# Optimization experiments

Measured on AMD Instinct MI355X. Metric: run time of the kernel, lower is better.

Reference implementation:

```python
import jax, jax.numpy as jnp
import numpy as np

B, N, K_NBR = 8, 4096, 16
H1, H3 = 512, 64
NS = 24  # covariance neighborhood size (hardcoded in encode)


def _local_cov(pc, ns):
    # Vectorized equivalent of the per-point sliding-window covariance loop.
    Bv, Nv, D = pc.shape
    half = ns // 2
    offs = jnp.arange(-half, half + 1)              # window size ns+1 = 25
    idx = jnp.arange(Nv)[:, None] + offs            # [N, 25]
    valid = (idx >= 0) & (idx < Nv)
    nb = pc[:, jnp.clip(idx, 0, Nv - 1), :]         # [B, N, 25, D]
    vm = valid[None, :, :, None].astype(pc.dtype)
    cnt = valid.sum(-1).astype(pc.dtype)[None, :, None]  # actual window counts
    mean = (nb * vm).sum(2) / cnt                   # [B, N, D]
    cen = (nb - mean[:, :, None, :]) * vm           # mask after centering
    cov = jnp.einsum('bnwd,bnwe->bnde', cen, cen) / (ns - 1)  # torch divides by ns-1
    return cov.reshape(Bv, Nv, D * D)


def _gcn(h, src, dst, w, b):
    # torch_geometric GCNConv: add self-loops, sym-normalize, aggregate at dst.
    Nt = h.shape[0]
    loop = jnp.arange(Nt, dtype=src.dtype)
    s = jnp.concatenate([src, loop])
    d = jnp.concatenate([dst, loop])
    deg = jax.ops.segment_sum(jnp.ones_like(d, h.dtype), d, num_segments=Nt)
    dinv = jnp.where(deg > 0, jax.lax.rsqrt(deg), 0.0)
    hw = h @ w
    msg = (dinv[s] * dinv[d])[:, None] * hw[s]
    return jax.ops.segment_sum(msg, d, num_segments=Nt) + b


def setup_inputs() -> dict:
    key = jax.random.key(0)
    ks = jax.random.split(key, 10)

    def lin(k, fi, fo):
        w = jax.random.normal(k, (fi, fo), jnp.float32) / np.float32(np.sqrt(fi))
        return w, jnp.zeros((fo,), jnp.float32)

    x = jax.random.normal(ks[0], (B, N, 3), jnp.float32)
    knn = jax.random.randint(ks[1], (2, B * N * K_NBR), 0, B * N, jnp.int32)
    w_e1, b_e1 = lin(ks[2], 12, H3)
    w_g1, b_g1 = lin(ks[3], H3, 2 * H3)
    w_g2, b_g2 = lin(ks[4], 2 * H3, H1)
    w_e2, b_e2 = lin(ks[5], H1, H1)
    w_d1, b_d1 = lin(ks[6], H1 + 2, 3)
    w_d2, b_d2 = lin(ks[7], H1 + 3, 3)
    return dict(x=x, knn=knn, w_e1=w_e1, b_e1=b_e1, w_g1=w_g1, b_g1=b_g1,
                w_g2=w_g2, b_g2=b_g2, w_e2=w_e2, b_e2=b_e2,
                w_d1=w_d1, b_d1=b_d1, w_d2=w_d2, b_d2=b_d2)


def reference(x, knn, w_e1, b_e1, w_g1, b_g1, w_g2, b_g2,
              w_e2, b_e2, w_d1, b_d1, w_d2, b_d2):
    act = jax.nn.selu
    Bv, Nv, _ = x.shape
    # ---- encode ----
    cov = _local_cov(x, NS)                                  # [B, N, 9]
    h = act(jnp.concatenate([x, cov], -1) @ w_e1 + b_e1)     # [B, N, H3]
    h = h.reshape(Bv * Nv, -1)
    h = act(_gcn(h, knn[0], knn[1], w_g1, b_g1))             # [B*N, 2*H3]
    h = act(_gcn(h, knn[0], knn[1], w_g2, b_g2))             # [B*N, H1]
    h = h.reshape(Bv, Nv, -1)
    lat = h.max(axis=1, keepdims=True)                       # AdaptiveMaxPool1d(1)
    lat = act(lat @ w_e2 + b_e2)                             # [B, 1, H1]
    # ---- decode ----
    nx = int(1 + (Nv * 120 / 60) ** 0.5)
    ny = int(1 + (Nv * 60 / 120) ** 0.5)
    xg = jnp.linspace(1.0, 120.0, nx)
    yg = jnp.linspace(1.0, 60.0, ny)
    grid = jnp.stack(jnp.meshgrid(xg, yg, indexing='ij'), -1).reshape(-1, 2)[:Nv]
    y = jnp.broadcast_to(grid[None], (Bv, Nv, 2))
    xr = jnp.broadcast_to(lat, (Bv, Nv, lat.shape[-1]))      # repeat codeword
    k = act(jnp.concatenate([xr, y], -1) @ w_d1 + b_d1)      # [B, N, 3]
    out = act(jnp.concatenate([xr, k], -1) @ w_d2 + b_d2)    # [B, N, 3]
    return out
```

## Files before the change

### kernel.cpp

```cpp
#include <hip/hip_runtime.h>
#include <math.h>

#define SELU_SCALE 1.0507009873554804934193349852946f
#define SELU_ALPHA 1.6732632423543772848170429916717f

typedef short bf16x8 __attribute__((ext_vector_type(8)));
typedef float f32x4 __attribute__((ext_vector_type(4)));

__device__ __forceinline__ float selu_f(float x) {
    return SELU_SCALE * (x > 0.f ? x : SELU_ALPHA * expm1f(x));
}

__device__ __forceinline__ unsigned short f2bf(float f) {
    unsigned int u = __float_as_uint(f);
    u += 0x7FFF + ((u >> 16) & 1);
    return (unsigned short)(u >> 16);
}
__device__ __forceinline__ float bflo(unsigned int u) { return __uint_as_float(u << 16); }
__device__ __forceinline__ float bfhi(unsigned int u) { return __uint_as_float(u & 0xFFFF0000u); }

__device__ __forceinline__ void acc8(float* a, uint4 v) {
    a[0] += bflo(v.x); a[1] += bfhi(v.x);
    a[2] += bflo(v.y); a[3] += bfhi(v.y);
    a[4] += bflo(v.z); a[5] += bfhi(v.z);
    a[6] += bflo(v.w); a[7] += bfhi(v.w);
}

__device__ __forceinline__ uint4 pack8(const float* a, float dv) {
    uint4 pk;
    pk.x = (unsigned int)f2bf(a[0] * dv) | ((unsigned int)f2bf(a[1] * dv) << 16);
    pk.y = (unsigned int)f2bf(a[2] * dv) | ((unsigned int)f2bf(a[3] * dv) << 16);
    pk.z = (unsigned int)f2bf(a[4] * dv) | ((unsigned int)f2bf(a[5] * dv) << 16);
    pk.w = (unsigned int)f2bf(a[6] * dv) | ((unsigned int)f2bf(a[7] * dv) << 16);
    return pk;
}

__global__ __launch_bounds__(256) void prep_kernel(
    int* __restrict__ cnt, unsigned int* __restrict__ pad1,
    unsigned int* __restrict__ pad2,
    const float* __restrict__ W1, unsigned short* __restrict__ Wp1,
    const float* __restrict__ W2, unsigned short* __restrict__ Wp2) {
    int b = blockIdx.x;
    int t = threadIdx.x;
    if (b < 128) {
        cnt[b * 256 + t] = 0;
    } else if (b == 128) {
        if (t < 32) pad1[t] = 0;
        if (t < 64) pad2[t] = 0;
    } else {
        if (t >= 64) return;
        int fb = b - 129;
        const float* W; unsigned short* Wp; int K, N, f;
        if (fb < 16) { W = W1; Wp = Wp1; K = 64; N = 128; f = fb; }
        else         { W = W2; Wp = Wp2; K = 128; N = 512; f = fb - 16; }
        int l = t;
        int KS = K / 32;
        int nt = f / KS, ks = f % KS;
        int ncol = nt * 16 + (l & 15);
        int k0 = ks * 32 + (l >> 4) * 8;
        unsigned short v[8];
        #pragma unroll
        for (int j = 0; j < 8; j++) v[j] = f2bf(W[(size_t)(k0 + j) * N + ncol]);
        *(uint4*)&Wp[((size_t)f * 64 + l) * 8] = *(uint4*)v;
    }
}

__global__ void count_kernel(const int* __restrict__ dst, int* __restrict__ cnt,
                             int* __restrict__ epos, int E) {
    int e = blockIdx.x * blockDim.x + threadIdx.x;
    if (e < E) epos[e] = atomicAdd(&cnt[dst[e]], 1);
}

__global__ __launch_bounds__(256) void scanA_kernel(const int* __restrict__ cnt,
                                                    int* __restrict__ blockSums) {
    __shared__ int red[256];
    int t = threadIdx.x;
    int c = cnt[blockIdx.x * 256 + t];
    red[t] = (c + 7) & ~7;
    __syncthreads();
    for (int s = 128; s > 0; s >>= 1) {
        if (t < s) red[t] += red[t + s];
        __syncthreads();
    }
    if (t == 0) blockSums[blockIdx.x] = red[0];
}

__global__ __launch_bounds__(256) void scanC_kernel(
    const int* __restrict__ cnt, const int* __restrict__ bsums,
    int* __restrict__ indptr, float* __restrict__ dinv, int* __restrict__ ssrc, int n) {
    __shared__ int sc[256];
    __shared__ int bs[128];
    int t = threadIdx.x;
    int ownSum = bsums[blockIdx.x];
    if (t < 128) bs[t] = bsums[t];
    int i = blockIdx.x * 256 + t;
    int c = cnt[i];
    int pc = (c + 7) & ~7;
    sc[t] = pc;
    __syncthreads();
    for (int off = 1; off < 128; off <<= 1) {
        int v = (t >= off && t < 128) ? bs[t - off] : 0;
        __syncthreads();
        if (t < 128) bs[t] += v;
        __syncthreads();
    }
    for (int off = 1; off < 256; off <<= 1) {
        int v = t >= off ? sc[t - off] : 0;
        __syncthreads();
        sc[t] += v;
        __syncthreads();
    }
    int blockOff = bs[blockIdx.x] - ownSum;
    int ip = blockOff + sc[t] - pc;
    indptr[i] = ip;
    dinv[i] = rsqrtf((float)(c + 1));
    for (int k = c; k < pc; k++) ssrc[ip + k] = n;
    if (i == n - 1) indptr[n] = blockOff + sc[t];
}

__global__ void scatter_kernel(const int* __restrict__ src, const int* __restrict__ dst,
                               const int* __restrict__ epos,
                               const int* __restrict__ indptr,
                               int* __restrict__ ssrc, int E) {
    int e = blockIdx.x * blockDim.x + threadIdx.x;
    if (e < E) ssrc[indptr[dst[e]] + epos[e]] = src[e];
}

__global__ __launch_bounds__(256) void cov_enc_kernel(
    const float* __restrict__ x, const float* __restrict__ w_e1,
    const float* __restrict__ b_e1, const float* __restrict__ dinv,
    unsigned short* __restrict__ hs1, int BN) {
    __shared__ float Wl[12 * 64];
    __shared__ float Bl[64];
    __shared__ float xs[280 * 3];
    int t = threadIdx.x;
    for (int i = t; i < 768; i += 256) Wl[i] = w_e1[i];
    if (t < 64) Bl[t] = b_e1[t];
    int p0 = blockIdx.x * 256;
    int n0 = p0 & 4095;
    const float* xb = x + (size_t)(p0 - n0) * 3;
    for (int idx = t; idx < 840; idx += 256) {
        int slot = idx / 3, d = idx - slot * 3;
        int g = n0 - 12 + slot;
        g = g < 0 ? 0 : (g > 4095 ? 4095 : g);
        xs[idx] = xb[g * 3 + d];
    }
    __syncthreads();
    int p = p0 + t;
    int n = n0 + t;
    int lo = n - 12 < 0 ? 0 : n - 12;
    int hi = n + 12 > 4095 ? 4095 : n + 12;
    int slo = lo - n0 + 12, shi = hi - n0 + 12;
    float sx = 0.f, sy = 0.f, sz = 0.f;
    float sxx = 0.f, sxy = 0.f, sxz = 0.f, syy = 0.f, syz = 0.f, szz = 0.f;
    for (int s = slo; s <= shi; s++) {
        float xv = xs[s * 3 + 0], yv = xs[s * 3 + 1], zv = xs[s * 3 + 2];
        sx += xv; sy += yv; sz += zv;
        sxx = fmaf(xv, xv, sxx); sxy = fmaf(xv, yv, sxy); sxz = fmaf(xv, zv, sxz);
        syy = fmaf(yv, yv, syy); syz = fmaf(yv, zv, syz); szz = fmaf(zv, zv, szz);
    }
    float cntf = (float)(shi - slo + 1);
    float rin = 1.f / cntf;
    float mx = sx * rin, my = sy * rin, mz = sz * rin;
    const float inv23 = 1.f / 23.f;
    float c00 = (sxx - sx * mx) * inv23;
    float c01 = (sxy - sx * my) * inv23;
    float c02 = (sxz - sx * mz) * inv23;
    float c11 = (syy - sy * my) * inv23;
    float c12 = (syz - sy * mz) * inv23;
    float c22 = (szz - sz * mz) * inv23;
    float feat[12];
    feat[0] = xs[(t + 12) * 3 + 0];
    feat[1] = xs[(t + 12) * 3 + 1];
    feat[2] = xs[(t + 12) * 3 + 2];
    feat[3] = c00; feat[4] = c01; feat[5]  = c02;
    feat[6] = c01; feat[7] = c11; feat[8]  = c12;
    feat[9] = c02; feat[10] = c12; feat[11] = c22;
    float dv = dinv[p];
    unsigned int* hp = (unsigned int*)(hs1 + (size_t)p * 64);
    for (int c = 0; c < 64; c += 2) {
        float a0 = Bl[c], a1 = Bl[c + 1];
        #pragma unroll
        for (int i = 0; i < 12; i++) {
            a0 = fmaf(feat[i], Wl[i * 64 + c], a0);
            a1 = fmaf(feat[i], Wl[i * 64 + c + 1], a1);
        }
        unsigned int pk = (unsigned int)f2bf(dv * selu_f(a0)) |
                          ((unsigned int)f2bf(dv * selu_f(a1)) << 16);
        hp[c >> 1] = pk;
    }
}

__global__ __launch_bounds__(256) void gcn1_kernel(
    const unsigned short* __restrict__ hs1, const float* __restrict__ dinv,
    const int* __restrict__ indptr, const int* __restrict__ ssrc,
    const unsigned short* __restrict__ Wp, const float* __restrict__ bias,
    unsigned short* __restrict__ hs2) {
    constexpr int LDA = 72;
    __shared__ unsigned short As[128 * LDA];
    int t = threadIdx.x;
    int R0 = blockIdx.x * 128;
    const uint4* hp = (const uint4*)hs1;

    for (int idx = t; idx < 1024; idx += 256) {
        int nl = idx >> 3, cq = idx & 7;
        int node = R0 + nl;
        float a[8];
        {
            uint4 u = hp[(size_t)node * 8 + cq];
            a[0] = bflo(u.x); a[1] = bfhi(u.x);
            a[2] = bflo(u.y); a[3] = bfhi(u.y);
            a[4] = bflo(u.z); a[5] = bfhi(u.z);
            a[6] = bflo(u.w); a[7] = bfhi(u.w);
        }
        int beg = indptr[node], end = indptr[node + 1];
        for (int j = beg; j < end; j += 8) {
            int s[8];
            #pragma unroll
            for (int q = 0; q < 8; q++) s[q] = ssrc[j + q];
            uint4 v[8];
            #pragma unroll
            for (int q = 0; q < 8; q++) v[q] = hp[(size_t)s[q] * 8 + cq];
            #pragma unroll
            for (int q = 0; q < 8; q++) acc8(a, v[q]);
        }
        *(uint4*)&As[nl * LDA + cq * 8] = pack8(a, dinv[node]);
    }
    __syncthreads();

    int wave = t >> 6, l = t & 63;
    int ml = l & 15, q = l >> 4;
    int wr = wave * 32;
    f32x4 acc[2][8];
    #pragma unroll
    for (int mf = 0; mf < 2; mf++)
        #pragma unroll
        for (int nf = 0; nf < 8; nf++) acc[mf][nf] = (f32x4){0.f, 0.f, 0.f, 0.f};
    const bf16x8* wp8 = (const bf16x8*)Wp;
    #pragma unroll
    for (int ks = 0; ks < 2; ks++) {
        bf16x8 af[2];
        #pragma unroll
        for (int mf = 0; mf < 2; mf++)
            af[mf] = *(const bf16x8*)&As[(wr + mf * 16 + ml) * LDA + ks * 32 + q * 8];
        bf16x8 bfr[8];
        #pragma unroll
        for (int nf = 0; nf < 8; nf++)
            bfr[nf] = wp8[(size_t)(nf * 2 + ks) * 64 + l];
        #pragma unroll
        for (int mf = 0; mf < 2; mf++)
            #pragma unroll
            for (int nf = 0; nf < 8; nf++)
                acc[mf][nf] = __builtin_amdgcn_mfma_f32_16x16x32_bf16(
                    af[mf], bfr[nf], acc[mf][nf], 0, 0, 0);
    }
    float bj[8];
    #pragma unroll
    for (int nf = 0; nf < 8; nf++) bj[nf] = bias[nf * 16 + ml];
    #pragma unroll
    for (int mf = 0; mf < 2; mf++) {
        #pragma unroll
        for (int r = 0; r < 4; r++) {
            int row = R0 + wr + mf * 16 + q * 4 + r;
            float dv = dinv[row];
            #pragma unroll
            for (int nf = 0; nf < 8; nf++) {
                float v = dv * selu_f(acc[mf][nf][r] + bj[nf]);
                hs2[(size_t)row * 128 + nf * 16 + ml] = f2bf(v);
            }
        }
    }
}

__global__ __launch_bounds__(256) void agg128_kernel(
    const unsigned short* __restrict__ hs, const float* __restrict__ dinv,
    const int* __restrict__ indptr, const int* __restrict__ ssrc,
    unsigned short* __restrict__ out, int n_nodes) {
    constexpr int TPN = 16;
    int node = blockIdx.x * (256 / TPN) + threadIdx.x / TPN;
    int cq = threadIdx.x % TPN;
    if (node >= n_nodes) return;
    const uint4* hp = (const uint4*)hs;
    float a[8];
    {
        uint4 u = hp[(size_t)node * TPN + cq];
        a[0] = bflo(u.x); a[1] = bfhi(u.x);
        a[2] = bflo(u.y); a[3] = bfhi(u.y);
        a[4] = bflo(u.z); a[5] = bfhi(u.z);
        a[6] = bflo(u.w); a[7] = bfhi(u.w);
    }
    int beg = indptr[node], end = indptr[node + 1];
    for (int j = beg; j < end; j += 8) {
        int s[8];
        #pragma unroll
        for (int q = 0; q < 8; q++) s[q] = ssrc[j + q];
        uint4 v[8];
        #pragma unroll
        for (int q = 0; q < 8; q++) v[q] = hp[(size_t)s[q] * TPN + cq];
        #pragma unroll
        for (int q = 0; q < 8; q++) acc8(a, v[q]);
    }
    ((uint4*)out)[(size_t)node * TPN + cq] = pack8(a, dinv[node]);
}

__global__ __launch_bounds__(256) void gemm2_kernel(
    const unsigned short* __restrict__ A, const unsigned short* __restrict__ Wp,
    const float* __restrict__ bias, float* __restrict__ pmax, int Nfull) {
    constexpr int KS = 4;
    constexpr int LDA = 136;
    constexpr int CPR = 16;
    __shared__ unsigned short As[128 * LDA];
    int t = threadIdx.x;
    int wave = t >> 6, l = t & 63;
    int ml = l & 15, q = l >> 4;
    int R0 = blockIdx.x * 128;
    int cb = blockIdx.y * 128;

    for (int c = t; c < 128 * CPR; c += 256) {
        int row = c / CPR, off = c % CPR;
        *(uint4*)&As[row * LDA + off * 8] =
            *(const uint4*)&A[(size_t)(R0 + row) * 128 + off * 8];
    }
    __syncthreads();

    f32x4 acc[2][8];
    #pragma unroll
    for (int mf = 0; mf < 2; mf++)
        #pragma unroll
        for (int nf = 0; nf < 8; nf++) acc[mf][nf] = (f32x4){0.f, 0.f, 0.f, 0.f};

    const bf16x8* wp8 = (const bf16x8*)Wp;
    int wr = wave * 32;
    #pragma unroll
    for (int ks = 0; ks < KS; ks++) {
        bf16x8 af[2];
        #pragma unroll
        for (int mf = 0; mf < 2; mf++)
            af[mf] = *(const bf16x8*)&As[(wr + mf * 16 + ml) * LDA + ks * 32 + q * 8];
        bf16x8 bfr[8];
        #pragma unroll
        for (int nf = 0; nf < 8; nf++)
            bfr[nf] = wp8[(size_t)(((cb >> 4) + nf) * KS + ks) * 64 + l];
        #pragma unroll
        for (int mf = 0; mf < 2; mf++)
            #pragma unroll
            for (int nf = 0; nf < 8; nf++)
                acc[mf][nf] = __builtin_amdgcn_mfma_f32_16x16x32_bf16(
                    af[mf], bfr[nf], acc[mf][nf], 0, 0, 0);
    }

    float cmax[8];
    #pragma unroll
    for (int nf = 0; nf < 8; nf++) {
        float bj = bias[cb + nf * 16 + ml];
        float v = -INFINITY;
        #pragma unroll
        for (int mf = 0; mf < 2; mf++)
            #pragma unroll
            for (int r = 0; r < 4; r++)
                v = fmaxf(v, selu_f(acc[mf][nf][r] + bj));
        v = fmaxf(v, __shfl_xor(v, 16, 64));
        v = fmaxf(v, __shfl_xor(v, 32, 64));
        cmax[nf] = v;
    }
    __syncthreads();
    float* redf = (float*)As;
    if (ml == l) {
        #pragma unroll
        for (int nf = 0; nf < 8; nf++) redf[wave * 128 + nf * 16 + l] = cmax[nf];
    }
    __syncthreads();
    if (t < 128) {
        float v = redf[t];
        v = fmaxf(v, redf[128 + t]);
        v = fmaxf(v, redf[256 + t]);
        v = fmaxf(v, redf[384 + t]);
        pmax[(size_t)blockIdx.x * Nfull + cb + t] = v;
    }
}

__global__ __launch_bounds__(256) void lat_kernel(
    const float* __restrict__ pmax, const float* __restrict__ w_e2,
    const float* __restrict__ b_e2, const float* __restrict__ w_d1,
    const float* __restrict__ b_d1, const float* __restrict__ w_d2,
    const float* __restrict__ b_d2, float* __restrict__ latw1,
    float* __restrict__ latw2) {
    int b = blockIdx.x;
    int t = threadIdx.x;
    __shared__ float ml[512], ll[512];
    __shared__ float red[6][256];
    for (int c = t; c < 512; c += 256) {
        const float* p = pmax + (size_t)(b * 32) * 512 + c;
        float v = -INFINITY;
        #pragma unroll
        for (int k = 0; k < 32; k++) v = fmaxf(v, p[k * 512]);
        ml[c] = v;
    }
    __syncthreads();
    for (int cc = 0; cc < 2; cc++) {
        int c = t + cc * 256;
        float acc = b_e2[c];
        for (int k = 0; k < 512; k++) acc = fmaf(ml[k], w_e2[k * 512 + c], acc);
        ll[c] = selu_f(acc);
    }
    __syncthreads();
    float p[6] = {0.f, 0.f, 0.f, 0.f, 0.f, 0.f};
    for (int k = t; k < 512; k += 256) {
        float lv = ll[k];
        #pragma unroll
        for (int j = 0; j < 3; j++) {
            p[j]     = fmaf(lv, w_d1[k * 3 + j], p[j]);
            p[3 + j] = fmaf(lv, w_d2[k * 3 + j], p[3 + j]);
        }
    }
    #pragma unroll
    for (int j = 0; j < 6; j++) red[j][t] = p[j];
    __syncthreads();
    for (int s = 128; s > 0; s >>= 1) {
        if (t < s) {
            #pragma unroll
            for (int j = 0; j < 6; j++) red[j][t] += red[j][t + s];
        }
        __syncthreads();
    }
    if (t < 3) {
        latw1[b * 3 + t] = red[t][0] + b_d1[t];
        latw2[b * 3 + t] = red[3 + t][0] + b_d2[t];
    }
}

__global__ void decode_kernel(const float* __restrict__ latw1, const float* __restrict__ latw2,
                              const float* __restrict__ w_d1, const float* __restrict__ w_d2,
                              float* __restrict__ out, int total) {
    int p = blockIdx.x * blockDim.x + threadIdx.x;
    if (p >= total) return;
    int b = p >> 12;
    int n = p & 4095;
    int i = n / 46;
    int j = n - i * 46;
    float y0 = fmaf((float)i, 119.f / 90.f, 1.f);
    float y1 = fmaf((float)j, 59.f / 45.f, 1.f);
    float k0 = selu_f(latw1[b * 3 + 0] + y0 * w_d1[1536 + 0] + y1 * w_d1[1539 + 0]);
    float k1 = selu_f(latw1[b * 3 + 1] + y0 * w_d1[1536 + 1] + y1 * w_d1[1539 + 1]);
    float k2 = selu_f(latw1[b * 3 + 2] + y0 * w_d1[1536 + 2] + y1 * w_d1[1539 + 2]);
    float o0 = selu_f(latw2[b * 3 + 0] + k0 * w_d2[1536 + 0] + k1 * w_d2[1539 + 0] + k2 * w_d2[1542 + 0]);
    float o1 = selu_f(latw2[b * 3 + 1] + k0 * w_d2[1536 + 1] + k1 * w_d2[1539 + 1] + k2 * w_d2[1542 + 1]);
    float o2 = selu_f(latw2[b * 3 + 2] + k0 * w_d2[1536 + 2] + k1 * w_d2[1539 + 2] + k2 * w_d2[1542 + 2]);
    out[(size_t)p * 3 + 0] = o0;
    out[(size_t)p * 3 + 1] = o1;
    out[(size_t)p * 3 + 2] = o2;
}

extern "C" void kernel_launch(void* const* d_in, const int* in_sizes, int n_in,
                              void* d_out, int out_size, void* d_ws, size_t ws_size,
                              hipStream_t stream) {
    const float* x    = (const float*)d_in[0];
    const int*   knn  = (const int*)d_in[1];
    const float* w_e1 = (const float*)d_in[2];
    const float* b_e1 = (const float*)d_in[3];
    const float* w_g1 = (const float*)d_in[4];
    const float* b_g1 = (const float*)d_in[5];
    const float* w_g2 = (const float*)d_in[6];
    const float* b_g2 = (const float*)d_in[7];
    const float* w_e2 = (const float*)d_in[8];
    const float* b_e2 = (const float*)d_in[9];
    const float* w_d1 = (const float*)d_in[10];
    const float* b_d1 = (const float*)d_in[11];
    const float* w_d2 = (const float*)d_in[12];
    const float* b_d2 = (const float*)d_in[13];
    float* out = (float*)d_out;

    const int BN = in_sizes[0] / 3;
    const int E  = in_sizes[1] / 2;
    const int Bb = BN / 4096;
    const int* src = knn;
    const int* dst = knn + E;

    size_t off = 0;
    auto alloc = [&](size_t bytes) -> void* {
        void* p = (char*)d_ws + off;
        off += (bytes + 255) & ~(size_t)255;
        return p;
    };
    unsigned short* hs1 = (unsigned short*)alloc((size_t)(BN + 1) * 64 * 2);
    unsigned short* hs2 = (unsigned short*)alloc((size_t)(BN + 1) * 128 * 2);
    unsigned short* a2  = (unsigned short*)alloc((size_t)BN * 128 * 2);
    unsigned short* Wp1 = (unsigned short*)alloc((size_t)16 * 64 * 8 * 2);
    unsigned short* Wp2 = (unsigned short*)alloc((size_t)128 * 64 * 8 * 2);
    float* pmax   = (float*)alloc((size_t)(BN / 128) * 512 * 4);
    float* latw1  = (float*)alloc((size_t)Bb * 3 * 4);
    float* latw2  = (float*)alloc((size_t)Bb * 3 * 4);
    float* dinv   = (float*)alloc((size_t)BN * 4);
    int*   cnt    = (int*)alloc((size_t)BN * 4);
    int*   epos   = (int*)alloc((size_t)E * 4);
    int*   indptr = (int*)alloc((size_t)(BN + 1) * 4);
    int*   bsums  = (int*)alloc((size_t)128 * 4);
    int*   ssrc   = (int*)alloc((size_t)(E + 7 * BN + 1024) * 4);
    (void)ws_size;

    prep_kernel<<<273, 256, 0, stream>>>(
        cnt, (unsigned int*)(hs1 + (size_t)BN * 64),
        (unsigned int*)(hs2 + (size_t)BN * 128), w_g1, Wp1, w_g2, Wp2);
    count_kernel<<<(E + 255) / 256, 256, 0, stream>>>(dst, cnt, epos, E);
    scanA_kernel<<<BN / 256, 256, 0, stream>>>(cnt, bsums);
    scanC_kernel<<<BN / 256, 256, 0, stream>>>(cnt, bsums, indptr, dinv, ssrc, BN);
    scatter_kernel<<<(E + 255) / 256, 256, 0, stream>>>(src, dst, epos, indptr, ssrc, E);

    cov_enc_kernel<<<(BN + 255) / 256, 256, 0, stream>>>(x, w_e1, b_e1, dinv, hs1, BN);

    gcn1_kernel<<<BN / 128, 256, 0, stream>>>(hs1, dinv, indptr, ssrc, Wp1, b_g1, hs2);

    agg128_kernel<<<BN / 16, 256, 0, stream>>>(hs2, dinv, indptr, ssrc, a2, BN);
    gemm2_kernel<<<dim3(BN / 128, 4), 256, 0, stream>>>(a2, Wp2, b_g2, pmax, 512);

    lat_kernel<<<Bb, 256, 0, stream>>>(pmax, w_e2, b_e2, w_d1, b_d1, w_d2, b_d2, latw1, latw2);

    decode_kernel<<<(BN + 255) / 256, 256, 0, stream>>>(latw1, latw2, w_d1, w_d2, out, BN);
}
```

Before: 236.1 us.

## Fuse GCN2 aggregation with GEMM+maxpool and merge scatter with covariance encode

Fuses the second GCN layer's neighbor aggregation into the GEMM kernel. Each block aggregates 64 nodes straight into LDS and then computes all 512 output columns with MFMA plus the per-block max, so the intermediate a2 buffer never goes to global memory. It also merges the edge-scatter and covariance-encode launches into one grid split by block index, and moves the dinv computation into scanA. The trade-offs are more accumulator registers (32 f32x4 per thread, launch bounds 256,2), lower aggregation parallelism per block, and twice as many pmax partials for lat_kernel to reduce.

```diff
diff --git a/kernel.cpp b/kernel.cpp
--- a/kernel.cpp
+++ b/kernel.cpp
@@ -72,10 +72,13 @@
 }
 
 __global__ __launch_bounds__(256) void scanA_kernel(const int* __restrict__ cnt,
-                                                    int* __restrict__ blockSums) {
+                                                    int* __restrict__ blockSums,
+                                                    float* __restrict__ dinv) {
     __shared__ int red[256];
     int t = threadIdx.x;
-    int c = cnt[blockIdx.x * 256 + t];
+    int i = blockIdx.x * 256 + t;
+    int c = cnt[i];
+    dinv[i] = rsqrtf((float)(c + 1));
     red[t] = (c + 7) & ~7;
     __syncthreads();
     for (int s = 128; s > 0; s >>= 1) {
@@ -87,7 +90,7 @@
 
 __global__ __launch_bounds__(256) void scanC_kernel(
     const int* __restrict__ cnt, const int* __restrict__ bsums,
-    int* __restrict__ indptr, float* __restrict__ dinv, int* __restrict__ ssrc, int n) {
+    int* __restrict__ indptr, int* __restrict__ ssrc, int n) {
     __shared__ int sc[256];
     __shared__ int bs[128];
     int t = threadIdx.x;
@@ -113,30 +116,30 @@
     int blockOff = bs[blockIdx.x] - ownSum;
     int ip = blockOff + sc[t] - pc;
     indptr[i] = ip;
-    dinv[i] = rsqrtf((float)(c + 1));
     for (int k = c; k < pc; k++) ssrc[ip + k] = n;
     if (i == n - 1) indptr[n] = blockOff + sc[t];
 }
 
-__global__ void scatter_kernel(const int* __restrict__ src, const int* __restrict__ dst,
-                               const int* __restrict__ epos,
-                               const int* __restrict__ indptr,
-                               int* __restrict__ ssrc, int E) {
-    int e = blockIdx.x * blockDim.x + threadIdx.x;
-    if (e < E) ssrc[indptr[dst[e]] + epos[e]] = src[e];
-}
-
-__global__ __launch_bounds__(256) void cov_enc_kernel(
+__global__ __launch_bounds__(256) void scatter_cov_kernel(
+    const int* __restrict__ src, const int* __restrict__ dst,
+    const int* __restrict__ epos, const int* __restrict__ indptr,
+    int* __restrict__ ssrc, int E, int nb_scatter,
     const float* __restrict__ x, const float* __restrict__ w_e1,
     const float* __restrict__ b_e1, const float* __restrict__ dinv,
-    unsigned short* __restrict__ hs1, int BN) {
+    unsigned short* __restrict__ hs1) {
+    int t = threadIdx.x;
+    if ((int)blockIdx.x < nb_scatter) {
+        int e = blockIdx.x * 256 + t;
+        if (e < E) ssrc[indptr[dst[e]] + epos[e]] = src[e];
+        return;
+    }
     __shared__ float Wl[12 * 64];
     __shared__ float Bl[64];
     __shared__ float xs[280 * 3];
-    int t = threadIdx.x;
+    int cb = blockIdx.x - nb_scatter;
     for (int i = t; i < 768; i += 256) Wl[i] = w_e1[i];
     if (t < 64) Bl[t] = b_e1[t];
-    int p0 = blockIdx.x * 256;
+    int p0 = cb * 256;
     int n0 = p0 & 4095;
     const float* xb = x + (size_t)(p0 - n0) * 3;
     for (int idx = t; idx < 840; idx += 256) {
@@ -272,110 +275,91 @@
     }
 }
 
-__global__ __launch_bounds__(256) void agg128_kernel(
-    const unsigned short* __restrict__ hs, const float* __restrict__ dinv,
+__global__ __launch_bounds__(256, 2) void gcn2_kernel(
+    const unsigned short* __restrict__ hs2, const float* __restrict__ dinv,
     const int* __restrict__ indptr, const int* __restrict__ ssrc,
-    unsigned short* __restrict__ out, int n_nodes) {
-    constexpr int TPN = 16;
-    int node = blockIdx.x * (256 / TPN) + threadIdx.x / TPN;
-    int cq = threadIdx.x % TPN;
-    if (node >= n_nodes) return;
-    const uint4* hp = (const uint4*)hs;
-    float a[8];
-    {
-        uint4 u = hp[(size_t)node * TPN + cq];
-        a[0] = bflo(u.x); a[1] = bfhi(u.x);
-        a[2] = bflo(u.y); a[3] = bfhi(u.y);
-        a[4] = bflo(u.z); a[5] = bfhi(u.z);
-        a[6] = bflo(u.w); a[7] = bfhi(u.w);
-    }
-    int beg = indptr[node], end = indptr[node + 1];
-    for (int j = beg; j < end; j += 8) {
-        int s[8];
-        #pragma unroll
-        for (int q = 0; q < 8; q++) s[q] = ssrc[j + q];
-        uint4 v[8];
-        #pragma unroll
-        for (int q = 0; q < 8; q++) v[q] = hp[(size_t)s[q] * TPN + cq];
-        #pragma unroll
-        for (int q = 0; q < 8; q++) acc8(a, v[q]);
-    }
-    ((uint4*)out)[(size_t)node * TPN + cq] = pack8(a, dinv[node]);
-}
-
-__global__ __launch_bounds__(256) void gemm2_kernel(
-    const unsigned short* __restrict__ A, const unsigned short* __restrict__ Wp,
-    const float* __restrict__ bias, float* __restrict__ pmax, int Nfull) {
-    constexpr int KS = 4;
+    const unsigned short* __restrict__ Wp, const float* __restrict__ bias,
+    float* __restrict__ pmax) {
     constexpr int LDA = 136;
-    constexpr int CPR = 16;
-    __shared__ unsigned short As[128 * LDA];
-    int t = threadIdx.x;
+    __shared__ unsigned short As[64 * LDA];
+    int t = threadIdx.x;
+    int R0 = blockIdx.x * 64;
+    const uint4* hp = (const uint4*)hs2;
+
+    #pragma unroll
+    for (int it = 0; it < 4; it++) {
+        int idx = it * 256 + t;
+        int half = idx >> 9;
+        int j9 = idx & 511;
+        int nl = j9 >> 3;
+        int cq = (half << 3) | (j9 & 7);
+        int node = R0 + nl;
+        float a[8];
+        {
+            uint4 u = hp[(size_t)node * 16 + cq];
+            a[0] = bflo(u.x); a[1] = bfhi(u.x);
+            a[2] = bflo(u.y); a[3] = bfhi(u.y);
+            a[4] = bflo(u.z); a[5] = bfhi(u.z);
+            a[6] = bflo(u.w); a[7] = bfhi(u.w);
+        }
+        int beg = indptr[node], end = indptr[node + 1];
+        for (int j = beg; j < end; j += 8) {
+            int s[8];
+            #pragma unroll
+            for (int q = 0; q < 8; q++) s[q] = ssrc[j + q];
+            uint4 v[8];
+            #pragma unroll
+            for (int q = 0; q < 8; q++) v[q] = hp[(size_t)s[q] * 16 + cq];
+            #pragma unroll
+            for (int q = 0; q < 8; q++) acc8(a, v[q]);
+        }
+        *(uint4*)&As[nl * LDA + cq * 8] = pack8(a, dinv[node]);
+    }
+    __syncthreads();
+
     int wave = t >> 6, l = t & 63;
     int ml = l & 15, q = l >> 4;
-    int R0 = blockIdx.x * 128;
-    int cb = blockIdx.y * 128;
-
-    for (int c = t; c < 128 * CPR; c += 256) {
-        int row = c / CPR, off = c % CPR;
-        *(uint4*)&As[row * LDA + off * 8] =
-            *(const uint4*)&A[(size_t)(R0 + row) * 128 + off * 8];
-    }
-    __syncthreads();
-
-    f32x4 acc[2][8];
-    #pragma unroll
-    for (int mf = 0; mf < 2; mf++)
-        #pragma unroll
-        for (int nf = 0; nf < 8; nf++) acc[mf][nf] = (f32x4){0.f, 0.f, 0.f, 0.f};
-
+    int wr = wave * 16;
+    f32x4 acc[32];
+    #pragma unroll
+    for (int nf = 0; nf < 32; nf++) acc[nf] = (f32x4){0.f, 0.f, 0.f, 0.f};
     const bf16x8* wp8 = (const bf16x8*)Wp;
-    int wr = wave * 32;
-    #pragma unroll
-    for (int ks = 0; ks < KS; ks++) {
-        bf16x8 af[2];
-        #pragma unroll
-        for (int mf = 0; mf < 2; mf++)
-            af[mf] = *(const bf16x8*)&As[(wr + mf * 16 + ml) * LDA + ks * 32 + q * 8];
-        bf16x8 bfr[8];
-        #pragma unroll
-        for (int nf = 0; nf < 8; nf++)
-            bfr[nf] = wp8[(size_t)(((cb >> 4) + nf) * KS + ks) * 64 + l];
-        #pragma unroll
-        for (int mf = 0; mf < 2; mf++)
-            #pragma unroll
-            for (int nf = 0; nf < 8; nf++)
-                acc[mf][nf] = __builtin_amdgcn_mfma_f32_16x16x32_bf16(
-                    af[mf], bfr[nf], acc[mf][nf], 0, 0, 0);
-    }
-
-    float cmax[8];
-    #pragma unroll
-    for (int nf = 0; nf < 8; nf++) {
-        float bj = bias[cb + nf * 16 + ml];
+    #pragma unroll
+    for (int ks = 0; ks < 4; ks++) {
+        bf16x8 af = *(const bf16x8*)&As[(wr + ml) * LDA + ks * 32 + q * 8];
+        #pragma unroll
+        for (int nf = 0; nf < 32; nf++) {
+            bf16x8 bfr = wp8[(size_t)(nf * 4 + ks) * 64 + l];
+            acc[nf] = __builtin_amdgcn_mfma_f32_16x16x32_bf16(af, bfr, acc[nf], 0, 0, 0);
+        }
+    }
+
+    float cmax[32];
+    #pragma unroll
+    for (int nf = 0; nf < 32; nf++) {
+        float bj = bias[nf * 16 + ml];
         float v = -INFINITY;
         #pragma unroll
-        for (int mf = 0; mf < 2; mf++)
-            #pragma unroll
-            for (int r = 0; r < 4; r++)
-                v = fmaxf(v, selu_f(acc[mf][nf][r] + bj));
+        for (int r = 0; r < 4; r++) v = fmaxf(v, selu_f(acc[nf][r] + bj));
         v = fmaxf(v, __shfl_xor(v, 16, 64));
         v = fmaxf(v, __shfl_xor(v, 32, 64));
         cmax[nf] = v;
     }
     __syncthreads();
     float* redf = (float*)As;
-    if (ml == l) {
-        #pragma unroll
-        for (int nf = 0; nf < 8; nf++) redf[wave * 128 + nf * 16 + l] = cmax[nf];
-    }
-    __syncthreads();
-    if (t < 128) {
-        float v = redf[t];
-        v = fmaxf(v, redf[128 + t]);
-        v = fmaxf(v, redf[256 + t]);
-        v = fmaxf(v, redf[384 + t]);
-        pmax[(size_t)blockIdx.x * Nfull + cb + t] = v;
+    if (l < 16) {
+        #pragma unroll
+        for (int nf = 0; nf < 32; nf++) redf[wave * 512 + nf * 16 + l] = cmax[nf];
+    }
+    __syncthreads();
+    #pragma unroll
+    for (int cc = 0; cc < 2; cc++) {
+        int c = cc * 256 + t;
+        float v = redf[c];
+        v = fmaxf(v, redf[512 + c]);
+        v = fmaxf(v, redf[1024 + c]);
+        v = fmaxf(v, redf[1536 + c]);
+        pmax[(size_t)blockIdx.x * 512 + c] = v;
     }
 }
 
@@ -390,10 +374,10 @@
     __shared__ float ml[512], ll[512];
     __shared__ float red[6][256];
     for (int c = t; c < 512; c += 256) {
-        const float* p = pmax + (size_t)(b * 32) * 512 + c;
+        const float* p = pmax + (size_t)(b * 64) * 512 + c;
         float v = -INFINITY;
         #pragma unroll
-        for (int k = 0; k < 32; k++) v = fmaxf(v, p[k * 512]);
+        for (int k = 0; k < 64; k++) v = fmaxf(v, p[k * 512]);
         ml[c] = v;
     }
     __syncthreads();
@@ -484,10 +468,9 @@
     };
     unsigned short* hs1 = (unsigned short*)alloc((size_t)(BN + 1) * 64 * 2);
     unsigned short* hs2 = (unsigned short*)alloc((size_t)(BN + 1) * 128 * 2);
-    unsigned short* a2  = (unsigned short*)alloc((size_t)BN * 128 * 2);
     unsigned short* Wp1 = (unsigned short*)alloc((size_t)16 * 64 * 8 * 2);
     unsigned short* Wp2 = (unsigned short*)alloc((size_t)128 * 64 * 8 * 2);
-    float* pmax   = (float*)alloc((size_t)(BN / 128) * 512 * 4);
+    float* pmax   = (float*)alloc((size_t)(BN / 64) * 512 * 4);
     float* latw1  = (float*)alloc((size_t)Bb * 3 * 4);
     float* latw2  = (float*)alloc((size_t)Bb * 3 * 4);
     float* dinv   = (float*)alloc((size_t)BN * 4);
@@ -498,20 +481,21 @@
     int*   ssrc   = (int*)alloc((size_t)(E + 7 * BN + 1024) * 4);
     (void)ws_size;
 
+    const int nb_scatter = (E + 255) / 256;
+
     prep_kernel<<<273, 256, 0, stream>>>(
         cnt, (unsigned int*)(hs1 + (size_t)BN * 64),
         (unsigned int*)(hs2 + (size_t)BN * 128), w_g1, Wp1, w_g2, Wp2);
     count_kernel<<<(E + 255) / 256, 256, 0, stream>>>(dst, cnt, epos, E);
-    scanA_kernel<<<BN / 256, 256, 0, stream>>>(cnt, bsums);
-    scanC_kernel<<<BN / 256, 256, 0, stream>>>(cnt, bsums, indptr, dinv, ssrc, BN);
-    scatter_kernel<<<(E + 255) / 256, 256, 0, stream>>>(src, dst, epos, indptr, ssrc, E);
-
-    cov_enc_kernel<<<(BN + 255) / 256, 256, 0, stream>>>(x, w_e1, b_e1, dinv, hs1, BN);
+    scanA_kernel<<<BN / 256, 256, 0, stream>>>(cnt, bsums, dinv);
+    scanC_kernel<<<BN / 256, 256, 0, stream>>>(cnt, bsums, indptr, ssrc, BN);
+    scatter_cov_kernel<<<nb_scatter + 128, 256, 0, stream>>>(
+        src, dst, epos, indptr, ssrc, E, nb_scatter,
+        x, w_e1, b_e1, dinv, hs1);
 
     gcn1_kernel<<<BN / 128, 256, 0, stream>>>(hs1, dinv, indptr, ssrc, Wp1, b_g1, hs2);
 
-    agg128_kernel<<<BN / 16, 256, 0, stream>>>(hs2, dinv, indptr, ssrc, a2, BN);
-    gemm2_kernel<<<dim3(BN / 128, 4), 256, 0, stream>>>(a2, Wp2, b_g2, pmax, 512);
+    gcn2_kernel<<<BN / 64, 256, 0, stream>>>(hs2, dinv, indptr, ssrc, Wp2, b_g2, pmax);
 
     lat_kernel<<<Bb, 256, 0, stream>>>(pmax, w_e2, b_e2, w_d1, b_d1, w_d2, b_d2, latw1, latw2);
 
```

Result: slower. 250.6 us (+6.1%).
